# Kernel tuning notes

Hardware: AMD Instinct MI355X
Metric: run time of the kernel (lower is better)

## Reference

```python
import jax, jax.numpy as jnp
import numpy as np

N_NODES = 100000
N_EDGES = 3200000
IN_CH, HID, OUT_CH = 256, 64, 64


def setup_inputs() -> dict:
    key = jax.random.key(0)
    k1, k2, k3, k4 = jax.random.split(key, 4)
    x = jax.random.normal(k1, (N_NODES, IN_CH), dtype=jnp.float32)
    edge_index = jax.random.randint(k2, (2, N_EDGES), 0, N_NODES, dtype=jnp.int64)
    W1 = jax.random.normal(k3, (IN_CH, HID), dtype=jnp.float32) * (1.0 / np.sqrt(IN_CH))
    b1 = jnp.zeros((HID,), dtype=jnp.float32)
    W2 = jax.random.normal(k4, (HID, OUT_CH), dtype=jnp.float32) * (1.0 / np.sqrt(HID))
    b2 = jnp.zeros((OUT_CH,), dtype=jnp.float32)
    return {"x": x, "edge_index": edge_index, "W1": W1, "b1": b1, "W2": W2, "b2": b2}


def reference(x, edge_index, W1, b1, W2, b2):
    N = x.shape[0]
    # GCN normalization: add self-loops, deg^{-1/2} on both endpoints
    loops = jnp.arange(N, dtype=edge_index.dtype)
    src = jnp.concatenate([edge_index[0], loops])
    dst = jnp.concatenate([edge_index[1], loops])
    deg = jax.ops.segment_sum(jnp.ones(src.shape, x.dtype), dst, num_segments=N)
    dinv = jnp.where(deg > 0, jax.lax.rsqrt(deg), 0.0)
    norm = dinv[src] * dinv[dst]  # [E+N]

    def gcn(h, W, b):
        h = h @ W  # dense linear transform
        # gather-scale-scatter aggregation over edges
        agg = jax.ops.segment_sum(h[src] * norm[:, None], dst, num_segments=N)
        return agg + b

    h = jax.nn.relu(gcn(x, W1, b1))
    return gcn(h, W2, b2)
```

## Files before the change

### kernel.cpp

```cpp
#include <hip/hip_runtime.h>

typedef unsigned short u16;
typedef unsigned int u32;
typedef __bf16 bf16x8 __attribute__((ext_vector_type(8)));
typedef float f32x4 __attribute__((ext_vector_type(4)));
typedef u16 u16x8 __attribute__((ext_vector_type(8)));

#define IN_CH 256
#define HID 64
#define BSHIFT 8
#define BNODES 256
#define NBUK 391
#define BCAP 10240
#define TILE 8192

__device__ __forceinline__ u16 f2bf(float f) {
  union { float f; unsigned u; } v; v.f = f;
  unsigned r = v.u + 0x7FFFu + ((v.u >> 16) & 1u);
  return (u16)(r >> 16);
}
__device__ __forceinline__ float bf2f(u16 h) {
  union { unsigned u; float f; } v; v.u = ((unsigned)h) << 16;
  return v.f;
}

__global__ void k_wprep(const float* __restrict__ W1, const float* __restrict__ W2,
                        u16* __restrict__ w1t, u16* __restrict__ w2t) {
  int t = blockIdx.x * blockDim.x + threadIdx.x;
  if (t < 64 * 256) {
    int n = t >> 8, k = t & 255;
    w1t[t] = f2bf(W1[k * 64 + n]);
  }
  int t2 = t - 64 * 256;
  if (t2 >= 0 && t2 < 64 * 64) {
    int n = t2 >> 6, k = t2 & 63;
    w2t[t2] = f2bf(W2[k * 64 + n]);
  }
}


__global__ __launch_bounds__(1024) void k_part(const int* __restrict__ e_src,
                                               const int* __restrict__ e_dst,
                                               int* __restrict__ bcnt,
                                               u32* __restrict__ bedge, int E) {
  __shared__ int lcnt[512];
  __shared__ int lscan[512];
  __shared__ int gbase[512];
  __shared__ int wsum[8];
  __shared__ u32 stag[TILE];
  __shared__ int dest[TILE];
  int t = threadIdx.x;
  int base = blockIdx.x * TILE;
  int here = E - base; if (here > TILE) here = TILE;

  if (t < 512) lcnt[t] = 0;
  __syncthreads();

  u32 m[8]; int bk[8]; int rk[8];
#pragma unroll
  for (int k = 0; k < 8; ++k) {
    int e = base + t + k * 1024;
    if (e < E) {
      int s = e_src[e], d = e_dst[e];
      bk[k] = d >> BSHIFT;
      m[k] = (u32)s | ((u32)(d & (BNODES - 1)) << 20);
      rk[k] = atomicAdd(&lcnt[bk[k]], 1);
    } else bk[k] = -1;
  }
  __syncthreads();

  int lane = t & 63, w = t >> 6;
  int v = 0, x = 0;
  if (t < 512) { v = lcnt[t]; x = v; }
#pragma unroll
  for (int off = 1; off < 64; off <<= 1) {
    int y = __shfl_up(x, off);
    if (lane >= off) x += y;
  }
  if (t < 512 && lane == 63) wsum[w] = x;
  __syncthreads();
  if (t < 512) {
    int wo = 0;
    for (int i = 0; i < w; ++i) wo += wsum[i];
    lscan[t] = x - v + wo;
  }
  __syncthreads();

  if (t < NBUK) gbase[t] = t * BCAP + atomicAdd(&bcnt[t], lcnt[t]);
  __syncthreads();

#pragma unroll
  for (int k = 0; k < 8; ++k) {
    if (bk[k] >= 0) {
      int p = lscan[bk[k]] + rk[k];
      stag[p] = m[k];
      dest[p] = gbase[bk[k]] + rk[k];
    }
  }
  __syncthreads();

#pragma unroll
  for (int k = 0; k < 8; ++k) {
    int p = t + k * 1024;
    if (p < here) bedge[dest[p]] = stag[p];
  }
}


__global__ __launch_bounds__(1024) void k_sort(const int* __restrict__ bcnt,
                                               u32* __restrict__ bedge,
                                               int* __restrict__ rptr,
                                               int* __restrict__ rcnt,
                                               float* __restrict__ dinv, int N) {
  __shared__ u32 stag[BCAP];
  __shared__ int hist[BNODES];
  __shared__ int cur[BNODES];
  __shared__ int wsum4[4];
  int b = blockIdx.x, t = threadIdx.x;
  if (t < BNODES) hist[t] = 0;
  __syncthreads();
  int n = bcnt[b]; if (n > BCAP) n = BCAP;
  u32* be = bedge + (size_t)b * BCAP;

  for (int i = t; i < n; i += 1024) atomicAdd(&hist[be[i] >> 20], 1);
  __syncthreads();

  int lane = t & 63, w = t >> 6;
  int v = 0, x = 0;
  if (t < BNODES) { v = hist[t]; x = v; }
#pragma unroll
  for (int off = 1; off < 64; off <<= 1) {
    int y = __shfl_up(x, off);
    if (lane >= off) x += y;
  }
  if (t < BNODES && lane == 63) wsum4[w] = x;
  __syncthreads();
  if (t < BNODES) {
    int wo = 0;
    for (int i = 0; i < w; ++i) wo += wsum4[i];
    int ex = x - v + wo;
    cur[t] = ex;
    int node = (b << BSHIFT) + t;
    if (node < N) {
      rptr[node] = b * BCAP + ex;
      rcnt[node] = v;
      dinv[node] = rsqrtf((float)(v + 1));
    }
  }
  __syncthreads();

  for (int i = t; i < n; i += 1024) {
    u32 m = be[i];
    int p = atomicAdd(&cur[m >> 20], 1);
    stag[p] = m;
  }
  __syncthreads();

  for (int i = t; i < n; i += 1024) be[i] = stag[i];
}


__global__ __launch_bounds__(256) void k_gemm1(const float* __restrict__ x,
                                               const u16* __restrict__ w1t,
                                               const float* __restrict__ dinv,
                                               u16* __restrict__ h1) {
  int lane = threadIdx.x & 63;
  int wave = threadIdx.x >> 6;
  int rowbase = blockIdx.x * 16;
  int colbase = wave * 16;
  int mn = lane & 15, quad = lane >> 4;
  const float* arow = x + (size_t)(rowbase + mn) * IN_CH + quad * 8;
  const u16* brow = w1t + (colbase + mn) * IN_CH + quad * 8;

  float4 a[16];
#pragma unroll
  for (int kc = 0; kc < 8; ++kc) {
    a[2 * kc] = *(const float4*)(arow + kc * 32);
    a[2 * kc + 1] = *(const float4*)(arow + kc * 32 + 4);
  }
  u16x8 bfr[8];
#pragma unroll
  for (int kc = 0; kc < 8; ++kc) bfr[kc] = *(const u16x8*)(brow + kc * 32);

  f32x4 acc = {0.f, 0.f, 0.f, 0.f};
#pragma unroll
  for (int kc = 0; kc < 8; ++kc) {
    float4 a0 = a[2 * kc], a1 = a[2 * kc + 1];
    u16x8 au;
    au[0] = f2bf(a0.x); au[1] = f2bf(a0.y); au[2] = f2bf(a0.z); au[3] = f2bf(a0.w);
    au[4] = f2bf(a1.x); au[5] = f2bf(a1.y); au[6] = f2bf(a1.z); au[7] = f2bf(a1.w);
    acc = __builtin_amdgcn_mfma_f32_16x16x32_bf16(
        __builtin_bit_cast(bf16x8, au), __builtin_bit_cast(bf16x8, bfr[kc]), acc, 0, 0, 0);
  }
#pragma unroll
  for (int r = 0; r < 4; ++r) {
    int row = rowbase + quad * 4 + r;
    h1[(size_t)row * HID + colbase + mn] = f2bf(dinv[row] * acc[r]);
  }
}

__global__ __launch_bounds__(256) void k_gemm2(const u16* __restrict__ g1,
                                               const u16* __restrict__ w2t,
                                               const float* __restrict__ dinv,
                                               u16* __restrict__ h2) {
  int lane = threadIdx.x & 63;
  int wave = threadIdx.x >> 6;
  int rowbase = blockIdx.x * 16;
  int colbase = wave * 16;
  int mn = lane & 15, quad = lane >> 4;
  const u16* arow = g1 + (size_t)(rowbase + mn) * HID + quad * 8;
  const u16* brow = w2t + (colbase + mn) * HID + quad * 8;
  u16x8 au0 = *(const u16x8*)(arow);
  u16x8 au1 = *(const u16x8*)(arow + 32);
  u16x8 bu0 = *(const u16x8*)(brow);
  u16x8 bu1 = *(const u16x8*)(brow + 32);
  f32x4 acc = {0.f, 0.f, 0.f, 0.f};
  acc = __builtin_amdgcn_mfma_f32_16x16x32_bf16(
      __builtin_bit_cast(bf16x8, au0), __builtin_bit_cast(bf16x8, bu0), acc, 0, 0, 0);
  acc = __builtin_amdgcn_mfma_f32_16x16x32_bf16(
      __builtin_bit_cast(bf16x8, au1), __builtin_bit_cast(bf16x8, bu1), acc, 0, 0, 0);
#pragma unroll
  for (int r = 0; r < 4; ++r) {
    int row = rowbase + quad * 4 + r;
    h2[(size_t)row * HID + colbase + mn] = f2bf(dinv[row] * acc[r]);
  }
}


template <bool RELU, bool BF16OUT>
__global__ __launch_bounds__(256) void k_agg(const u16* __restrict__ hin,
                                             const int* __restrict__ rptr,
                                             const int* __restrict__ rcnt,
                                             const u32* __restrict__ sedge,
                                             const float* __restrict__ bias,
                                             void* __restrict__ outv, int N) {
  int wid = blockIdx.x * 4 + (threadIdx.x >> 6);
  int lane = threadIdx.x & 63;
  if (wid >= N) return;
  int start = __builtin_amdgcn_readfirstlane(rptr[wid]);
  int len = __builtin_amdgcn_readfirstlane(rcnt[wid]);
  float di = rsqrtf((float)(len + 1));
  float a0 = bf2f(hin[(size_t)wid * HID + lane]);
  float a1 = 0.f, a2 = 0.f, a3 = 0.f;
  const u32* se = sedge + start;
  int j = 0;
  for (; j + 16 <= len; j += 16) {
    u16 v[16];
#pragma unroll
    for (int k = 0; k < 16; ++k) {
      int e = (int)(se[j + k] & 0xFFFFF);
      v[k] = hin[(size_t)e * HID + lane];
    }
#pragma unroll
    for (int k = 0; k < 16; ++k) {
      float f = bf2f(v[k]);
      if ((k & 3) == 0) a0 += f;
      else if ((k & 3) == 1) a1 += f;
      else if ((k & 3) == 2) a2 += f;
      else a3 += f;
    }
  }
  if (j + 8 <= len) {
    u16 v[8];
#pragma unroll
    for (int k = 0; k < 8; ++k) {
      int e = (int)(se[j + k] & 0xFFFFF);
      v[k] = hin[(size_t)e * HID + lane];
    }
#pragma unroll
    for (int k = 0; k < 8; ++k) {
      float f = bf2f(v[k]);
      if ((k & 3) == 0) a0 += f;
      else if ((k & 3) == 1) a1 += f;
      else if ((k & 3) == 2) a2 += f;
      else a3 += f;
    }
    j += 8;
  }
  if (j + 4 <= len) {
    u16 v[4];
#pragma unroll
    for (int k = 0; k < 4; ++k) {
      int e = (int)(se[j + k] & 0xFFFFF);
      v[k] = hin[(size_t)e * HID + lane];
    }
    a0 += bf2f(v[0]); a1 += bf2f(v[1]); a2 += bf2f(v[2]); a3 += bf2f(v[3]);
    j += 4;
  }
  for (; j < len; ++j) {
    int e = (int)(se[j] & 0xFFFFF);
    a0 += bf2f(hin[(size_t)e * HID + lane]);
  }
  float acc = (a0 + a1) + (a2 + a3);
  acc = di * acc + bias[lane];
  if (RELU) acc = fmaxf(acc, 0.f);
  if (BF16OUT) ((u16*)outv)[(size_t)wid * HID + lane] = f2bf(acc);
  else ((float*)outv)[(size_t)wid * HID + lane] = acc;
}


extern "C" void kernel_launch(void* const* d_in, const int* in_sizes, int n_in,
                              void* d_out, int out_size, void* d_ws, size_t ws_size,
                              hipStream_t stream) {
  const float* x = (const float*)d_in[0];
  const int* ei = (const int*)d_in[1];
  const float* W1 = (const float*)d_in[2];
  const float* b1 = (const float*)d_in[3];
  const float* W2 = (const float*)d_in[4];
  const float* b2 = (const float*)d_in[5];
  float* out = (float*)d_out;

  const int N = in_sizes[0] / IN_CH;
  const int E = in_sizes[1] / 2;
  const int* e_src = ei;
  const int* e_dst = ei + E;

  size_t off = 0;
  auto carve = [&](size_t bytes) -> char* {
    char* p = (char*)d_ws + off;
    off += (bytes + 255) & ~(size_t)255;
    return p;
  };
  int* bcnt = (int*)carve((size_t)NBUK * 4);
  u32* bedge = (u32*)carve((size_t)NBUK * BCAP * 4);
  int* rptr = (int*)carve((size_t)N * 4);
  int* rcnt = (int*)carve((size_t)N * 4);
  float* dinv = (float*)carve((size_t)N * 4);
  u16* w1t = (u16*)carve(64 * 256 * 2);
  u16* w2t = (u16*)carve(64 * 64 * 2);
  u16* h1 = (u16*)carve((size_t)N * HID * 2);
  u16* g1 = (u16*)carve((size_t)N * HID * 2);

  const int n_tiles = (E + TILE - 1) / TILE;

  hipMemsetAsync(bcnt, 0, (size_t)NBUK * 4, stream);
  k_wprep<<<(64 * 256 + 64 * 64 + 255) / 256, 256, 0, stream>>>(W1, W2, w1t, w2t);
  k_part<<<n_tiles, 1024, 0, stream>>>(e_src, e_dst, bcnt, bedge, E);
  k_sort<<<NBUK, 1024, 0, stream>>>(bcnt, bedge, rptr, rcnt, dinv, N);
  k_gemm1<<<N / 16, 256, 0, stream>>>(x, w1t, dinv, h1);
  k_agg<true, true><<<(N + 3) / 4, 256, 0, stream>>>(h1, rptr, rcnt, bedge, b1, g1, N);
  k_gemm2<<<N / 16, 256, 0, stream>>>(g1, w2t, dinv, h1);
  k_agg<false, false><<<(N + 3) / 4, 256, 0, stream>>>(h1, rptr, rcnt, bedge, b2, out, N);
}
```

Before: 371.7 us.

## Have each gemm1 wave compute all 64 output columns for its own 16 rows

Before, the four waves of a block each loaded and converted the same 16 fp32 rows of x and computed a different 16-column slice. Now each wave owns its own 16 rows, converts the activations once, and loops over all four column tiles, reusing the A fragments across 32 MFMAs. This removes the 4x redundant reads and bf16 conversions of x, at the cost of more registers per wave. Launch bounds hints are also added to both gemm1 and the aggregation kernel.

```diff
diff --git a/kernel.cpp b/kernel.cpp
--- a/kernel.cpp
+++ b/kernel.cpp
@@ -160,17 +160,16 @@
 }
 
 
-__global__ __launch_bounds__(256) void k_gemm1(const float* __restrict__ x,
-                                               const u16* __restrict__ w1t,
-                                               const float* __restrict__ dinv,
-                                               u16* __restrict__ h1) {
+__global__ __launch_bounds__(256, 1) void k_gemm1(const float* __restrict__ x,
+                                                  const u16* __restrict__ w1t,
+                                                  const float* __restrict__ dinv,
+                                                  u16* __restrict__ h1, int N) {
   int lane = threadIdx.x & 63;
   int wave = threadIdx.x >> 6;
-  int rowbase = blockIdx.x * 16;
-  int colbase = wave * 16;
+  int rowbase = (blockIdx.x * 4 + wave) * 16;
+  if (rowbase >= N) return;
   int mn = lane & 15, quad = lane >> 4;
   const float* arow = x + (size_t)(rowbase + mn) * IN_CH + quad * 8;
-  const u16* brow = w1t + (colbase + mn) * IN_CH + quad * 8;
 
   float4 a[16];
 #pragma unroll
@@ -178,24 +177,37 @@
     a[2 * kc] = *(const float4*)(arow + kc * 32);
     a[2 * kc + 1] = *(const float4*)(arow + kc * 32 + 4);
   }
-  u16x8 bfr[8];
-#pragma unroll
-  for (int kc = 0; kc < 8; ++kc) bfr[kc] = *(const u16x8*)(brow + kc * 32);
-
-  f32x4 acc = {0.f, 0.f, 0.f, 0.f};
+  u16x8 au[8];
 #pragma unroll
   for (int kc = 0; kc < 8; ++kc) {
     float4 a0 = a[2 * kc], a1 = a[2 * kc + 1];
-    u16x8 au;
-    au[0] = f2bf(a0.x); au[1] = f2bf(a0.y); au[2] = f2bf(a0.z); au[3] = f2bf(a0.w);
-    au[4] = f2bf(a1.x); au[5] = f2bf(a1.y); au[6] = f2bf(a1.z); au[7] = f2bf(a1.w);
-    acc = __builtin_amdgcn_mfma_f32_16x16x32_bf16(
-        __builtin_bit_cast(bf16x8, au), __builtin_bit_cast(bf16x8, bfr[kc]), acc, 0, 0, 0);
+    au[kc][0] = f2bf(a0.x); au[kc][1] = f2bf(a0.y);
+    au[kc][2] = f2bf(a0.z); au[kc][3] = f2bf(a0.w);
+    au[kc][4] = f2bf(a1.x); au[kc][5] = f2bf(a1.y);
+    au[kc][6] = f2bf(a1.z); au[kc][7] = f2bf(a1.w);
+  }
+
+  f32x4 acc[4] = {{0.f, 0.f, 0.f, 0.f}, {0.f, 0.f, 0.f, 0.f},
+                  {0.f, 0.f, 0.f, 0.f}, {0.f, 0.f, 0.f, 0.f}};
+#pragma unroll
+  for (int c = 0; c < 4; ++c) {
+    const u16* brow = w1t + (c * 16 + mn) * IN_CH + quad * 8;
+    u16x8 bu[8];
+#pragma unroll
+    for (int kc = 0; kc < 8; ++kc) bu[kc] = *(const u16x8*)(brow + kc * 32);
+#pragma unroll
+    for (int kc = 0; kc < 8; ++kc)
+      acc[c] = __builtin_amdgcn_mfma_f32_16x16x32_bf16(
+          __builtin_bit_cast(bf16x8, au[kc]), __builtin_bit_cast(bf16x8, bu[kc]),
+          acc[c], 0, 0, 0);
   }
 #pragma unroll
   for (int r = 0; r < 4; ++r) {
     int row = rowbase + quad * 4 + r;
-    h1[(size_t)row * HID + colbase + mn] = f2bf(dinv[row] * acc[r]);
+    float dv = dinv[row];
+#pragma unroll
+    for (int c = 0; c < 4; ++c)
+      h1[(size_t)row * HID + c * 16 + mn] = f2bf(dv * acc[c][r]);
   }
 }
 
@@ -228,12 +240,12 @@
 
 
 template <bool RELU, bool BF16OUT>
-__global__ __launch_bounds__(256) void k_agg(const u16* __restrict__ hin,
-                                             const int* __restrict__ rptr,
-                                             const int* __restrict__ rcnt,
-                                             const u32* __restrict__ sedge,
-                                             const float* __restrict__ bias,
-                                             void* __restrict__ outv, int N) {
+__global__ __launch_bounds__(256, 4) void k_agg(const u16* __restrict__ hin,
+                                                const int* __restrict__ rptr,
+                                                const int* __restrict__ rcnt,
+                                                const u32* __restrict__ sedge,
+                                                const float* __restrict__ bias,
+                                                void* __restrict__ outv, int N) {
   int wid = blockIdx.x * 4 + (threadIdx.x >> 6);
   int lane = threadIdx.x & 63;
   if (wid >= N) return;
@@ -332,12 +344,13 @@
   u16* g1 = (u16*)carve((size_t)N * HID * 2);
 
   const int n_tiles = (E + TILE - 1) / TILE;
+  const int nb_g1 = (N + 63) / 64;
 
   hipMemsetAsync(bcnt, 0, (size_t)NBUK * 4, stream);
   k_wprep<<<(64 * 256 + 64 * 64 + 255) / 256, 256, 0, stream>>>(W1, W2, w1t, w2t);
   k_part<<<n_tiles, 1024, 0, stream>>>(e_src, e_dst, bcnt, bedge, E);
   k_sort<<<NBUK, 1024, 0, stream>>>(bcnt, bedge, rptr, rcnt, dinv, N);
-  k_gemm1<<<N / 16, 256, 0, stream>>>(x, w1t, dinv, h1);
+  k_gemm1<<<nb_g1, 256, 0, stream>>>(x, w1t, dinv, h1, N);
   k_agg<true, true><<<(N + 3) / 4, 256, 0, stream>>>(h1, rptr, rcnt, bedge, b1, g1, N);
   k_gemm2<<<N / 16, 256, 0, stream>>>(g1, w2t, dinv, h1);
   k_agg<false, false><<<(N + 3) / 4, 256, 0, stream>>>(h1, rptr, rcnt, bedge, b2, out, N);
```

Result: faster. 347.2 us (-6.6%).
